# Performance work log

Hardware: AMD Instinct MI355X
Metric: run time of the kernel (lower is better)

The kernel has to match this reference:

```python
import jax, jax.numpy as jnp
import numpy as np

EMBED_DIM = 768
NUM_HEADS = 12
HEAD_DIM = EMBED_DIM // NUM_HEADS
B, N = 4, 2048


def setup_inputs() -> dict:
    key = jax.random.key(0)
    k_x, k_wqkv, k_bqkv, k_wo, k_bo = jax.random.split(key, 5)
    s = 1.0 / np.sqrt(EMBED_DIM)
    return {
        "x": jax.random.normal(k_x, (B, N, EMBED_DIM), dtype=jnp.float32),
        # torch nn.Linear weight layout: [out_features, in_features]
        "w_qkv": jax.random.uniform(k_wqkv, (3 * EMBED_DIM, EMBED_DIM), minval=-s, maxval=s, dtype=jnp.float32),
        "b_qkv": jax.random.uniform(k_bqkv, (3 * EMBED_DIM,), minval=-s, maxval=s, dtype=jnp.float32),
        "w_out": jax.random.uniform(k_wo, (EMBED_DIM, EMBED_DIM), minval=-s, maxval=s, dtype=jnp.float32),
        "b_out": jax.random.uniform(k_bo, (EMBED_DIM,), minval=-s, maxval=s, dtype=jnp.float32),
    }


def reference(x, w_qkv, b_qkv, w_out, b_out):
    Bsz, Nlen, C = x.shape
    # fused QKV projection: [B, N, 3C]
    qkv = jnp.einsum("bnc,oc->bno", x, w_qkv) + b_qkv
    qkv = qkv.reshape(Bsz, Nlen, 3, NUM_HEADS, HEAD_DIM)
    q = qkv[:, :, 0].transpose(0, 2, 1, 3)  # [B, H, N, D]
    k = qkv[:, :, 1].transpose(0, 2, 1, 3)
    v = qkv[:, :, 2].transpose(0, 2, 1, 3)
    scale = 1.0 / np.sqrt(HEAD_DIM).astype(np.float32)
    scores = jnp.einsum("bhqd,bhkd->bhqk", q, k) * scale  # [B, H, N, N]
    attn = jax.nn.softmax(scores, axis=-1)
    ctx = jnp.einsum("bhqk,bhkd->bhqd", attn, v)  # [B, H, N, D]
    ctx = ctx.transpose(0, 2, 1, 3).reshape(Bsz, Nlen, C)
    return jnp.einsum("bnc,oc->bno", ctx, w_out) + b_out
```

## Files before the change

### kernel.cpp

```cpp
#include <hip/hip_runtime.h>
#include <math.h>

typedef __attribute__((ext_vector_type(8))) short bf16x8;
typedef __attribute__((ext_vector_type(4))) short bf16x4;
typedef __attribute__((ext_vector_type(4))) float f32x4;
typedef __attribute__((ext_vector_type(16))) float f32x16;
typedef unsigned short u16;

namespace {
constexpr int BATCH = 4, SEQ = 2048, CDIM = 768, NH = 12, HD = 64;
constexpr int MROWS = BATCH * SEQ;
constexpr int KD = CDIM;
constexpr float QSCALE = 0.125f * 1.44269504088896f;
}

__device__ __forceinline__ u16 f2bf(float f) {
  unsigned x = __float_as_uint(f);
  return (u16)((x + 0x7fffu + ((x >> 16) & 1u)) >> 16);
}

__device__ __forceinline__ unsigned pk2bf(float a, float b) {
  unsigned r;
  asm("v_cvt_pk_bf16_f32 %0, %1, %2" : "=v"(r) : "v"(a), "v"(b));
  return r;
}

#if defined(__has_builtin)
#if __has_builtin(__builtin_amdgcn_exp2f)
#define EXP2(x) __builtin_amdgcn_exp2f(x)
#endif
#endif
#ifndef EXP2
#define EXP2(x) exp2f(x)
#endif

#define GLD16(gp, lp)                                                        \
  __builtin_amdgcn_global_load_lds(                                          \
      (const __attribute__((address_space(1))) void*)(gp),                   \
      (__attribute__((address_space(3))) void*)(lp), 16, 0, 0)

__global__ void convert_bf16(const float* __restrict__ x, u16* __restrict__ xb, int nx4,
                             const float* __restrict__ w1, u16* __restrict__ w1b, int n14,
                             const float* __restrict__ w2, u16* __restrict__ w2b, int n24) {
  const int stride = gridDim.x * blockDim.x;
  const int t0 = blockIdx.x * blockDim.x + threadIdx.x;
  for (int i = t0; i < nx4; i += stride) {
    float4 v = ((const float4*)x)[i];
    ushort4 o; o.x = f2bf(v.x); o.y = f2bf(v.y); o.z = f2bf(v.z); o.w = f2bf(v.w);
    ((ushort4*)xb)[i] = o;
  }
  for (int i = t0; i < n14; i += stride) {
    float4 v = ((const float4*)w1)[i];
    ushort4 o; o.x = f2bf(v.x); o.y = f2bf(v.y); o.z = f2bf(v.z); o.w = f2bf(v.w);
    ((ushort4*)w1b)[i] = o;
  }
  for (int i = t0; i < n24; i += stride) {
    float4 v = ((const float4*)w2)[i];
    ushort4 o; o.x = f2bf(v.x); o.y = f2bf(v.y); o.z = f2bf(v.z); o.w = f2bf(v.w);
    ((ushort4*)w2b)[i] = o;
  }
}

template <int MODE>
__global__ __launch_bounds__(512, 4) void gemm_bf16(
    const u16* __restrict__ A, const u16* __restrict__ Bw,
    const float* __restrict__ bias, float* __restrict__ outf,
    u16* __restrict__ qws, u16* __restrict__ kws, u16* __restrict__ vws) {
  __shared__ u16 smem[2 * 2 * 128 * 64];
  const int t = threadIdx.x;
  const int w = t >> 6, l = t & 63, g = l >> 4, li = l & 15;
  const int wm = w >> 1, wn = w & 1;
  const int lin = blockIdx.x;
  const int rowb = ((lin & 7) << 3) | ((lin >> 3) & 7);
  const int colb = lin >> 6;
  const int row0 = rowb * 128, col0 = colb * 128;

  const int srow = w * 16 + (l >> 3);
  const int skc = (l & 7) ^ (l >> 3);
  const u16* gA = A + (size_t)(row0 + srow) * KD + skc * 8;
  const u16* gB = Bw + (size_t)(col0 + srow) * KD + skc * 8;

  f32x4 acc[2][4];
#pragma unroll
  for (int a = 0; a < 2; ++a)
#pragma unroll
    for (int c = 0; c < 4; ++c) acc[a][c] = {0.f, 0.f, 0.f, 0.f};

#define GSTAGE(kt_, buf_)                                                     \
  do {                                                                        \
    const int k0_ = (kt_) * 64;                                               \
    u16* As_ = smem + (buf_) * (2 * 128 * 64);                                \
    u16* Bs_ = As_ + 128 * 64;                                                \
    _Pragma("unroll")                                                         \
    for (int j = 0; j < 2; ++j) {                                             \
      GLD16(gA + (size_t)8 * j * KD + k0_, &As_[(w * 16 + 8 * j) * 64]);      \
      GLD16(gB + (size_t)8 * j * KD + k0_, &Bs_[(w * 16 + 8 * j) * 64]);      \
    }                                                                         \
  } while (0)

  constexpr int NK = KD / 64;
  GSTAGE(0, 0);
  GSTAGE(1, 1);
  asm volatile("s_waitcnt vmcnt(4)" ::: "memory");
  __builtin_amdgcn_sched_barrier(0);
  __builtin_amdgcn_s_barrier();
  __builtin_amdgcn_sched_barrier(0);

  for (int kt = 0; kt < NK; ++kt) {
    const int cur = kt & 1;
    const u16* AsC = smem + cur * (2 * 128 * 64);
    const u16* BsC = AsC + 128 * 64;

    bf16x8 af[2][2], bfr[4][2];
#pragma unroll
    for (int mi = 0; mi < 2; ++mi) {
      const int r = wm * 32 + mi * 16 + li;
#pragma unroll
      for (int ks = 0; ks < 2; ++ks)
        af[mi][ks] = *(const bf16x8*)&AsC[r * 64 + (((ks * 4 + g) ^ (li & 7)) * 8)];
    }
#pragma unroll
    for (int ni = 0; ni < 4; ++ni) {
      const int r = wn * 64 + ni * 16 + li;
#pragma unroll
      for (int ks = 0; ks < 2; ++ks)
        bfr[ni][ks] = *(const bf16x8*)&BsC[r * 64 + (((ks * 4 + g) ^ (li & 7)) * 8)];
    }
    __builtin_amdgcn_s_setprio(1);
#pragma unroll
    for (int ni = 0; ni < 4; ++ni)
#pragma unroll
      for (int mi = 0; mi < 2; ++mi) {
        acc[mi][ni] = __builtin_amdgcn_mfma_f32_16x16x32_bf16(af[mi][0], bfr[ni][0], acc[mi][ni], 0, 0, 0);
        acc[mi][ni] = __builtin_amdgcn_mfma_f32_16x16x32_bf16(af[mi][1], bfr[ni][1], acc[mi][ni], 0, 0, 0);
      }
    __builtin_amdgcn_s_setprio(0);

    if (kt + 1 < NK) {
      asm volatile("s_waitcnt vmcnt(0)" ::: "memory");
      __builtin_amdgcn_sched_barrier(0);
      __builtin_amdgcn_s_barrier();
      __builtin_amdgcn_sched_barrier(0);
      if (kt + 2 < NK) GSTAGE(kt + 2, cur);
    }
  }
#undef GSTAGE

  float bsr[4];
#pragma unroll
  for (int ni = 0; ni < 4; ++ni) bsr[ni] = bias[col0 + wn * 64 + ni * 16 + li];
  const int bidx = row0 >> 11;
  const int nseq0 = row0 & (SEQ - 1);

  __syncthreads();

  if (MODE == 1) {
    float* Cf = (float*)smem;
#pragma unroll
    for (int p = 0; p < 4; ++p) {
      if (wm == p) {
#pragma unroll
        for (int mi = 0; mi < 2; ++mi)
#pragma unroll
          for (int ni = 0; ni < 4; ++ni)
#pragma unroll
            for (int i = 0; i < 4; ++i)
              Cf[(mi * 16 + 4 * g + i) * 132 + wn * 64 + ni * 16 + li] =
                  acc[mi][ni][i] + bsr[ni];
      }
      __syncthreads();
#pragma unroll
      for (int j = 0; j < 2; ++j) {
        const int fid = t + 512 * j;
        const int r = fid >> 5, c4 = (fid & 31) * 4;
        *(float4*)(outf + (size_t)(row0 + p * 32 + r) * CDIM + col0 + c4) =
            *(const float4*)&Cf[r * 132 + c4];
      }
      __syncthreads();
    }
  } else {
#pragma unroll
    for (int hc = 0; hc < 2; ++hc) {
      const int nb = col0 + hc * 64;
      const int s = nb / CDIM;
      const int h = (nb % CDIM) / HD;
      if (wn == hc) {
        if (s < 2) {
          const float qs = (s == 0) ? QSCALE : 1.f;
#pragma unroll
          for (int mi = 0; mi < 2; ++mi)
#pragma unroll
            for (int ni = 0; ni < 4; ++ni)
#pragma unroll
              for (int i = 0; i < 4; ++i)
                smem[(wm * 32 + mi * 16 + 4 * g + i) * 72 + ni * 16 + li] =
                    f2bf((acc[mi][ni][i] + bsr[ni]) * qs);
        } else {
#pragma unroll
          for (int mi = 0; mi < 2; ++mi)
#pragma unroll
            for (int ni = 0; ni < 4; ++ni)
#pragma unroll
              for (int i = 0; i < 4; ++i)
                smem[(ni * 16 + li) * 136 + wm * 32 + mi * 16 + 4 * g + i] =
                    f2bf(acc[mi][ni][i] + bsr[ni]);
        }
      }
      __syncthreads();
      if (s < 2) {
        u16* dst = (s == 0 ? qws : kws) + ((size_t)(bidx * NH + h) * SEQ + nseq0) * HD;
        const int r = t >> 3, c = (t & 7) * 8;
#pragma unroll
        for (int rd = 0; rd < 2; ++rd)
          *(uint4*)(dst + (size_t)(r + 64 * rd) * HD + c) =
              *(const uint4*)&smem[(r + 64 * rd) * 72 + c];
      } else {
        u16* dst = vws + (size_t)(bidx * NH + h) * HD * SEQ + nseq0;
        const int d = t >> 4, c = (t & 15) * 8;
#pragma unroll
        for (int rd = 0; rd < 2; ++rd)
          *(uint4*)(dst + (size_t)(d + 32 * rd) * SEQ + c) =
              *(const uint4*)&smem[(d + 32 * rd) * 136 + c];
      }
      __syncthreads();
    }
  }
}

__global__ __launch_bounds__(128, 2) void attn_mfma(
    const u16* __restrict__ qws, const u16* __restrict__ kws,
    const u16* __restrict__ vws, u16* __restrict__ ctx) {
  __shared__ u16 smem[4 * 64 * 64];
  u16* Ks0 = smem;
  u16* Vs0 = smem + 2 * 64 * 64;
  const int t = threadIdx.x;
  const int w = t >> 6, l = t & 63;
  const int hi = l >> 5, c = l & 31;
  const int n = blockIdx.x;
  const int xcd = n & 7, j = n >> 3;
  const int hb = xcd * 6 + (j >> 4);
  const int q0 = (j & 15) * 128;
  const int h = hb % NH, b = hb / NH;
  const size_t bh = (size_t)b * NH + h;
  const u16* qbp = qws + bh * SEQ * HD;
  const u16* kb = kws + bh * SEQ * HD;
  const u16* vb = vws + bh * HD * SEQ;
  const int qw = q0 + w * 64;

  bf16x8 qf[2][4];
#pragma unroll
  for (int qt = 0; qt < 2; ++qt)
#pragma unroll
    for (int ks4 = 0; ks4 < 4; ++ks4)
      qf[qt][ks4] = *(const bf16x8*)(qbp + (size_t)(qw + qt * 32 + c) * HD + ks4 * 16 + hi * 8);
  asm volatile("s_waitcnt vmcnt(0)" ::: "memory");
  __builtin_amdgcn_sched_barrier(0);

  f32x16 acc[2][2];
#pragma unroll
  for (int dt = 0; dt < 2; ++dt)
#pragma unroll
    for (int qt = 0; qt < 2; ++qt)
#pragma unroll
      for (int r = 0; r < 16; ++r) acc[dt][qt][r] = 0.f;
  f32x16 Z;
#pragma unroll
  for (int r = 0; r < 16; ++r) Z[r] = 0.f;
  float lrun[2] = {0.f, 0.f};

  const int srow8 = l >> 3;
  const int skc = (l & 7) ^ srow8;
  const u16* gK = kb + (size_t)(w * 32 + srow8) * HD + skc * 8;
  const u16* gV = vb + (size_t)(w * 32 + srow8) * SEQ + skc * 8;

  constexpr int NT = SEQ / 64;

#define STAGE(kt_, buf_)                                                           \
  do {                                                                             \
    const int key0_ = (kt_) * 64;                                                  \
    _Pragma("unroll")                                                              \
    for (int jj = 0; jj < 4; ++jj) {                                               \
      GLD16(gK + (size_t)(key0_ + 8 * jj) * HD, &Ks0[(buf_) * 4096 + (w * 32 + 8 * jj) * 64]); \
      GLD16(gV + (size_t)(8 * jj) * SEQ + key0_, &Vs0[(buf_) * 4096 + (w * 32 + 8 * jj) * 64]); \
    }                                                                              \
  } while (0)

  STAGE(0, 0);
  STAGE(1, 1);
  asm volatile("s_waitcnt vmcnt(8)" ::: "memory");
  __builtin_amdgcn_sched_barrier(0);
  __builtin_amdgcn_s_barrier();
  __builtin_amdgcn_sched_barrier(0);

  for (int kt = 0; kt < NT; ++kt) {
    const int cur = kt & 1;
    const u16* KsC = Ks0 + cur * 4096;
    const u16* VsC = Vs0 + cur * 4096;

#pragma unroll
    for (int kt32 = 0; kt32 < 2; ++kt32) {
      f32x16 S0, S1;
      __builtin_amdgcn_s_setprio(1);
      {
        bf16x8 kf0 = *(const bf16x8*)&KsC[(kt32 * 32 + c) * 64 + (((0 * 2 + hi) ^ (l & 7)) * 8)];
        S0 = __builtin_amdgcn_mfma_f32_32x32x16_bf16(kf0, qf[0][0], Z, 0, 0, 0);
        S1 = __builtin_amdgcn_mfma_f32_32x32x16_bf16(kf0, qf[1][0], Z, 0, 0, 0);
        bf16x8 kf1 = *(const bf16x8*)&KsC[(kt32 * 32 + c) * 64 + (((1 * 2 + hi) ^ (l & 7)) * 8)];
        S0 = __builtin_amdgcn_mfma_f32_32x32x16_bf16(kf1, qf[0][1], S0, 0, 0, 0);
        S1 = __builtin_amdgcn_mfma_f32_32x32x16_bf16(kf1, qf[1][1], S1, 0, 0, 0);
        bf16x8 kf2 = *(const bf16x8*)&KsC[(kt32 * 32 + c) * 64 + (((2 * 2 + hi) ^ (l & 7)) * 8)];
        S0 = __builtin_amdgcn_mfma_f32_32x32x16_bf16(kf2, qf[0][2], S0, 0, 0, 0);
        S1 = __builtin_amdgcn_mfma_f32_32x32x16_bf16(kf2, qf[1][2], S1, 0, 0, 0);
        bf16x8 kf3 = *(const bf16x8*)&KsC[(kt32 * 32 + c) * 64 + (((3 * 2 + hi) ^ (l & 7)) * 8)];
        S0 = __builtin_amdgcn_mfma_f32_32x32x16_bf16(kf3, qf[0][3], S0, 0, 0, 0);
        S1 = __builtin_amdgcn_mfma_f32_32x32x16_bf16(kf3, qf[1][3], S1, 0, 0, 0);
      }
      __builtin_amdgcn_s_setprio(0);

      unsigned W0[4][2], W1[4][2];
#pragma unroll
      for (int qt = 0; qt < 2; ++qt) {
        const f32x16& S = (qt == 0) ? S0 : S1;
        float rs = 0.f;
#pragma unroll
        for (int u = 0; u < 4; ++u) {
          const float p0 = EXP2(S[4 * u + 0]);
          const float p1 = EXP2(S[4 * u + 1]);
          const float p2 = EXP2(S[4 * u + 2]);
          const float p3 = EXP2(S[4 * u + 3]);
          rs += (p0 + p1) + (p2 + p3);
          unsigned lo = pk2bf(p0, p1);
          unsigned hiw = pk2bf(p2, p3);
          if (qt == 0) { W0[u][0] = lo; W0[u][1] = hiw; }
          else         { W1[u][0] = lo; W1[u][1] = hiw; }
        }
        lrun[qt] += rs;
      }

      __builtin_amdgcn_s_setprio(1);
#pragma unroll
      for (int s = 0; s < 2; ++s) {
        union { uint4 u4; bf16x8 v; } p0v, p1v;
        p0v.u4.x = W0[2 * s][0]; p0v.u4.y = W0[2 * s][1];
        p0v.u4.z = W0[2 * s + 1][0]; p0v.u4.w = W0[2 * s + 1][1];
        p1v.u4.x = W1[2 * s][0]; p1v.u4.y = W1[2 * s][1];
        p1v.u4.z = W1[2 * s + 1][0]; p1v.u4.w = W1[2 * s + 1][1];
        const int ck0 = kt32 * 4 + 2 * s;
        const int ck1 = ck0 + 1;
#pragma unroll
        for (int dt = 0; dt < 2; ++dt) {
          const int rowoff = (dt * 32 + c) * 64;
          union { struct { bf16x4 a, b; } p; bf16x8 v; } vfu;
          vfu.p.a = *(const bf16x4*)&VsC[rowoff + ((ck0 ^ (l & 7)) * 8) + hi * 4];
          vfu.p.b = *(const bf16x4*)&VsC[rowoff + ((ck1 ^ (l & 7)) * 8) + hi * 4];
          acc[dt][0] = __builtin_amdgcn_mfma_f32_32x32x16_bf16(vfu.v, p0v.v, acc[dt][0], 0, 0, 0);
          acc[dt][1] = __builtin_amdgcn_mfma_f32_32x32x16_bf16(vfu.v, p1v.v, acc[dt][1], 0, 0, 0);
        }
      }
      __builtin_amdgcn_s_setprio(0);
    }

    if (kt + 1 < NT) {
      asm volatile("s_waitcnt vmcnt(0)" ::: "memory");
      __builtin_amdgcn_sched_barrier(0);
      __builtin_amdgcn_s_barrier();
      __builtin_amdgcn_sched_barrier(0);
      if (kt + 2 < NT) STAGE(kt + 2, cur);
    }
  }
#undef STAGE

  float inv[2];
#pragma unroll
  for (int qt = 0; qt < 2; ++qt) {
    lrun[qt] += __shfl_xor(lrun[qt], 32);
    inv[qt] = 1.f / lrun[qt];
  }
  __syncthreads();
  u16* Os = smem + w * (64 * 72);
#pragma unroll
  for (int qt = 0; qt < 2; ++qt)
#pragma unroll
    for (int dt = 0; dt < 2; ++dt)
#pragma unroll
      for (int u = 0; u < 4; ++u) {
        uint2 pk;
        pk.x = pk2bf(acc[dt][qt][4 * u + 0] * inv[qt], acc[dt][qt][4 * u + 1] * inv[qt]);
        pk.y = pk2bf(acc[dt][qt][4 * u + 2] * inv[qt], acc[dt][qt][4 * u + 3] * inv[qt]);
        const int row = qt * 32 + c;
        const int d0 = dt * 32 + 8 * u + 4 * hi;
        *(uint2*)&Os[row * 72 + d0] = pk;
      }
  asm volatile("s_waitcnt lgkmcnt(0)" ::: "memory");
  __builtin_amdgcn_sched_barrier(0);
  {
    const int rr = l >> 3, cc = (l & 7) * 8;
#pragma unroll
    for (int it = 0; it < 8; ++it) {
      const int row = 8 * it + rr;
      *(uint4*)(ctx + ((size_t)b * SEQ + qw + row) * CDIM + h * HD + cc) =
          *(const uint4*)&Os[row * 72 + cc];
    }
  }
}

extern "C" void kernel_launch(void* const* d_in, const int* in_sizes, int n_in,
                              void* d_out, int out_size, void* d_ws, size_t ws_size,
                              hipStream_t stream) {
  (void)in_sizes; (void)n_in; (void)out_size; (void)ws_size;
  const float* x     = (const float*)d_in[0];
  const float* w_qkv = (const float*)d_in[1];
  const float* b_qkv = (const float*)d_in[2];
  const float* w_out = (const float*)d_in[3];
  const float* b_out = (const float*)d_in[4];
  float* out = (float*)d_out;

  u16* xb    = (u16*)d_ws;
  u16* wqkvb = xb + (size_t)MROWS * KD;
  u16* wob   = wqkvb + (size_t)3 * CDIM * KD;
  u16* qb    = wob + (size_t)CDIM * KD;
  const size_t QS = (size_t)BATCH * NH * SEQ * HD;
  u16* kb   = qb + QS;
  u16* vb   = kb + QS;
  u16* ctxb = vb + QS;

  hipLaunchKernelGGL(convert_bf16, dim3(2048), dim3(256), 0, stream,
                     x, xb, MROWS * KD / 4,
                     w_qkv, wqkvb, 3 * CDIM * KD / 4,
                     w_out, wob, CDIM * KD / 4);
  hipLaunchKernelGGL((gemm_bf16<0>), dim3((MROWS / 128) * (3 * CDIM / 128)), dim3(512), 0,
                     stream, xb, wqkvb, b_qkv, nullptr, qb, kb, vb);
  hipLaunchKernelGGL(attn_mfma, dim3(16 * NH * BATCH), dim3(128), 0, stream,
                     qb, kb, vb, ctxb);
  hipLaunchKernelGGL((gemm_bf16<1>), dim3((MROWS / 128) * (CDIM / 128)), dim3(512), 0,
                     stream, ctxb, wob, b_out, out, nullptr, nullptr, nullptr);
}
```

Measured before the change: 207.6 us.

## Split attention key range across two wave pairs and reduce partials in LDS

The attention kernel goes from 128 to 256 threads per block. Two wave pairs each process half of the key sequence (split-K) for the same 128 queries, and their unnormalized accumulators and row sums are combined through shared memory at the end. Each iteration now handles 32 keys per wave pair instead of 64. The intent is more waves per CU to hide latency and shorter serial loops. The cost is an extra LDS reduction and barriers, plus more per-block register and LDS pressure.

```diff
diff --git a/kernel.cpp b/kernel.cpp
--- a/kernel.cpp
+++ b/kernel.cpp
@@ -227,15 +227,16 @@
   }
 }
 
-__global__ __launch_bounds__(128, 2) void attn_mfma(
+__global__ __launch_bounds__(256, 3) void attn_mfma(
     const u16* __restrict__ qws, const u16* __restrict__ kws,
     const u16* __restrict__ vws, u16* __restrict__ ctx) {
-  __shared__ u16 smem[4 * 64 * 64];
+  __shared__ u16 smem[16896];
   u16* Ks0 = smem;
-  u16* Vs0 = smem + 2 * 64 * 64;
+  u16* Vs0 = smem + 8192;
   const int t = threadIdx.x;
   const int w = t >> 6, l = t & 63;
   const int hi = l >> 5, c = l & 31;
+  const int kh = w >> 1, wq = w & 1;
   const int n = blockIdx.x;
   const int xcd = n & 7, j = n >> 3;
   const int hb = xcd * 6 + (j >> 4);
@@ -245,7 +246,7 @@
   const u16* qbp = qws + bh * SEQ * HD;
   const u16* kb = kws + bh * SEQ * HD;
   const u16* vb = vws + bh * HD * SEQ;
-  const int qw = q0 + w * 64;
+  const int qw = q0 + wq * 64;
 
   bf16x8 qf[2][4];
 #pragma unroll
@@ -270,24 +271,24 @@
 
   const int srow8 = l >> 3;
   const int skc = (l & 7) ^ srow8;
-  const u16* gK = kb + (size_t)(w * 32 + srow8) * HD + skc * 8;
-  const u16* gV = vb + (size_t)(w * 32 + srow8) * SEQ + skc * 8;
-
-  constexpr int NT = SEQ / 64;
-
-#define STAGE(kt_, buf_)                                                           \
+  const u16* gK = kb + (size_t)((w >> 1) * 1024 + (w & 1) * 16 + srow8) * HD + skc * 8;
+  const u16* gV = vb + (size_t)(w * 16 + srow8) * SEQ + (skc >> 2) * 1024 + (skc & 3) * 8;
+
+  constexpr int NT = SEQ / 2 / 32;
+
+#define STAGE(t_, buf_)                                                            \
   do {                                                                             \
-    const int key0_ = (kt_) * 64;                                                  \
+    const int key0_ = (t_) * 32;                                                   \
     _Pragma("unroll")                                                              \
-    for (int jj = 0; jj < 4; ++jj) {                                               \
-      GLD16(gK + (size_t)(key0_ + 8 * jj) * HD, &Ks0[(buf_) * 4096 + (w * 32 + 8 * jj) * 64]); \
-      GLD16(gV + (size_t)(8 * jj) * SEQ + key0_, &Vs0[(buf_) * 4096 + (w * 32 + 8 * jj) * 64]); \
+    for (int jj = 0; jj < 2; ++jj) {                                               \
+      GLD16(gK + (size_t)(key0_ + 8 * jj) * HD, &Ks0[(buf_) * 4096 + (w * 16 + 8 * jj) * 64]); \
+      GLD16(gV + (size_t)(8 * jj) * SEQ + key0_, &Vs0[(buf_) * 4096 + (w * 16 + 8 * jj) * 64]); \
     }                                                                              \
   } while (0)
 
   STAGE(0, 0);
   STAGE(1, 1);
-  asm volatile("s_waitcnt vmcnt(8)" ::: "memory");
+  asm volatile("s_waitcnt vmcnt(4)" ::: "memory");
   __builtin_amdgcn_sched_barrier(0);
   __builtin_amdgcn_s_barrier();
   __builtin_amdgcn_sched_barrier(0);
@@ -297,68 +298,65 @@
     const u16* KsC = Ks0 + cur * 4096;
     const u16* VsC = Vs0 + cur * 4096;
 
-#pragma unroll
-    for (int kt32 = 0; kt32 < 2; ++kt32) {
-      f32x16 S0, S1;
-      __builtin_amdgcn_s_setprio(1);
-      {
-        bf16x8 kf0 = *(const bf16x8*)&KsC[(kt32 * 32 + c) * 64 + (((0 * 2 + hi) ^ (l & 7)) * 8)];
-        S0 = __builtin_amdgcn_mfma_f32_32x32x16_bf16(kf0, qf[0][0], Z, 0, 0, 0);
-        S1 = __builtin_amdgcn_mfma_f32_32x32x16_bf16(kf0, qf[1][0], Z, 0, 0, 0);
-        bf16x8 kf1 = *(const bf16x8*)&KsC[(kt32 * 32 + c) * 64 + (((1 * 2 + hi) ^ (l & 7)) * 8)];
-        S0 = __builtin_amdgcn_mfma_f32_32x32x16_bf16(kf1, qf[0][1], S0, 0, 0, 0);
-        S1 = __builtin_amdgcn_mfma_f32_32x32x16_bf16(kf1, qf[1][1], S1, 0, 0, 0);
-        bf16x8 kf2 = *(const bf16x8*)&KsC[(kt32 * 32 + c) * 64 + (((2 * 2 + hi) ^ (l & 7)) * 8)];
-        S0 = __builtin_amdgcn_mfma_f32_32x32x16_bf16(kf2, qf[0][2], S0, 0, 0, 0);
-        S1 = __builtin_amdgcn_mfma_f32_32x32x16_bf16(kf2, qf[1][2], S1, 0, 0, 0);
-        bf16x8 kf3 = *(const bf16x8*)&KsC[(kt32 * 32 + c) * 64 + (((3 * 2 + hi) ^ (l & 7)) * 8)];
-        S0 = __builtin_amdgcn_mfma_f32_32x32x16_bf16(kf3, qf[0][3], S0, 0, 0, 0);
-        S1 = __builtin_amdgcn_mfma_f32_32x32x16_bf16(kf3, qf[1][3], S1, 0, 0, 0);
-      }
-      __builtin_amdgcn_s_setprio(0);
-
-      unsigned W0[4][2], W1[4][2];
-#pragma unroll
-      for (int qt = 0; qt < 2; ++qt) {
-        const f32x16& S = (qt == 0) ? S0 : S1;
-        float rs = 0.f;
-#pragma unroll
-        for (int u = 0; u < 4; ++u) {
-          const float p0 = EXP2(S[4 * u + 0]);
-          const float p1 = EXP2(S[4 * u + 1]);
-          const float p2 = EXP2(S[4 * u + 2]);
-          const float p3 = EXP2(S[4 * u + 3]);
-          rs += (p0 + p1) + (p2 + p3);
-          unsigned lo = pk2bf(p0, p1);
-          unsigned hiw = pk2bf(p2, p3);
-          if (qt == 0) { W0[u][0] = lo; W0[u][1] = hiw; }
-          else         { W1[u][0] = lo; W1[u][1] = hiw; }
-        }
-        lrun[qt] += rs;
-      }
-
-      __builtin_amdgcn_s_setprio(1);
-#pragma unroll
-      for (int s = 0; s < 2; ++s) {
-        union { uint4 u4; bf16x8 v; } p0v, p1v;
-        p0v.u4.x = W0[2 * s][0]; p0v.u4.y = W0[2 * s][1];
-        p0v.u4.z = W0[2 * s + 1][0]; p0v.u4.w = W0[2 * s + 1][1];
-        p1v.u4.x = W1[2 * s][0]; p1v.u4.y = W1[2 * s][1];
-        p1v.u4.z = W1[2 * s + 1][0]; p1v.u4.w = W1[2 * s + 1][1];
-        const int ck0 = kt32 * 4 + 2 * s;
-        const int ck1 = ck0 + 1;
-#pragma unroll
-        for (int dt = 0; dt < 2; ++dt) {
-          const int rowoff = (dt * 32 + c) * 64;
-          union { struct { bf16x4 a, b; } p; bf16x8 v; } vfu;
-          vfu.p.a = *(const bf16x4*)&VsC[rowoff + ((ck0 ^ (l & 7)) * 8) + hi * 4];
-          vfu.p.b = *(const bf16x4*)&VsC[rowoff + ((ck1 ^ (l & 7)) * 8) + hi * 4];
-          acc[dt][0] = __builtin_amdgcn_mfma_f32_32x32x16_bf16(vfu.v, p0v.v, acc[dt][0], 0, 0, 0);
-          acc[dt][1] = __builtin_amdgcn_mfma_f32_32x32x16_bf16(vfu.v, p1v.v, acc[dt][1], 0, 0, 0);
-        }
-      }
-      __builtin_amdgcn_s_setprio(0);
-    }
+    f32x16 S0, S1;
+    __builtin_amdgcn_s_setprio(1);
+    {
+      bf16x8 kf0 = *(const bf16x8*)&KsC[(kh * 32 + c) * 64 + (((0 * 2 + hi) ^ (l & 7)) * 8)];
+      S0 = __builtin_amdgcn_mfma_f32_32x32x16_bf16(kf0, qf[0][0], Z, 0, 0, 0);
+      S1 = __builtin_amdgcn_mfma_f32_32x32x16_bf16(kf0, qf[1][0], Z, 0, 0, 0);
+      bf16x8 kf1 = *(const bf16x8*)&KsC[(kh * 32 + c) * 64 + (((1 * 2 + hi) ^ (l & 7)) * 8)];
+      S0 = __builtin_amdgcn_mfma_f32_32x32x16_bf16(kf1, qf[0][1], S0, 0, 0, 0);
+      S1 = __builtin_amdgcn_mfma_f32_32x32x16_bf16(kf1, qf[1][1], S1, 0, 0, 0);
+      bf16x8 kf2 = *(const bf16x8*)&KsC[(kh * 32 + c) * 64 + (((2 * 2 + hi) ^ (l & 7)) * 8)];
+      S0 = __builtin_amdgcn_mfma_f32_32x32x16_bf16(kf2, qf[0][2], S0, 0, 0, 0);
+      S1 = __builtin_amdgcn_mfma_f32_32x32x16_bf16(kf2, qf[1][2], S1, 0, 0, 0);
+      bf16x8 kf3 = *(const bf16x8*)&KsC[(kh * 32 + c) * 64 + (((3 * 2 + hi) ^ (l & 7)) * 8)];
+      S0 = __builtin_amdgcn_mfma_f32_32x32x16_bf16(kf3, qf[0][3], S0, 0, 0, 0);
+      S1 = __builtin_amdgcn_mfma_f32_32x32x16_bf16(kf3, qf[1][3], S1, 0, 0, 0);
+    }
+    __builtin_amdgcn_s_setprio(0);
+
+    unsigned W0[4][2], W1[4][2];
+#pragma unroll
+    for (int qt = 0; qt < 2; ++qt) {
+      const f32x16& S = (qt == 0) ? S0 : S1;
+      float rs = 0.f;
+#pragma unroll
+      for (int u = 0; u < 4; ++u) {
+        const float p0 = EXP2(S[4 * u + 0]);
+        const float p1 = EXP2(S[4 * u + 1]);
+        const float p2 = EXP2(S[4 * u + 2]);
+        const float p3 = EXP2(S[4 * u + 3]);
+        rs += (p0 + p1) + (p2 + p3);
+        unsigned lo = pk2bf(p0, p1);
+        unsigned hiw = pk2bf(p2, p3);
+        if (qt == 0) { W0[u][0] = lo; W0[u][1] = hiw; }
+        else         { W1[u][0] = lo; W1[u][1] = hiw; }
+      }
+      lrun[qt] += rs;
+    }
+
+    __builtin_amdgcn_s_setprio(1);
+#pragma unroll
+    for (int s = 0; s < 2; ++s) {
+      union { uint4 u4; bf16x8 v; } p0v, p1v;
+      p0v.u4.x = W0[2 * s][0]; p0v.u4.y = W0[2 * s][1];
+      p0v.u4.z = W0[2 * s + 1][0]; p0v.u4.w = W0[2 * s + 1][1];
+      p1v.u4.x = W1[2 * s][0]; p1v.u4.y = W1[2 * s][1];
+      p1v.u4.z = W1[2 * s + 1][0]; p1v.u4.w = W1[2 * s + 1][1];
+      const int ck0 = kh * 4 + 2 * s;
+      const int ck1 = ck0 + 1;
+#pragma unroll
+      for (int dt = 0; dt < 2; ++dt) {
+        const int rowoff = (dt * 32 + c) * 64;
+        union { struct { bf16x4 a, b; } p; bf16x8 v; } vfu;
+        vfu.p.a = *(const bf16x4*)&VsC[rowoff + ((ck0 ^ (l & 7)) * 8) + hi * 4];
+        vfu.p.b = *(const bf16x4*)&VsC[rowoff + ((ck1 ^ (l & 7)) * 8) + hi * 4];
+        acc[dt][0] = __builtin_amdgcn_mfma_f32_32x32x16_bf16(vfu.v, p0v.v, acc[dt][0], 0, 0, 0);
+        acc[dt][1] = __builtin_amdgcn_mfma_f32_32x32x16_bf16(vfu.v, p1v.v, acc[dt][1], 0, 0, 0);
+      }
+    }
+    __builtin_amdgcn_s_setprio(0);
 
     if (kt + 1 < NT) {
       asm volatile("s_waitcnt vmcnt(0)" ::: "memory");
@@ -370,30 +368,56 @@
   }
 #undef STAGE
 
-  float inv[2];
-#pragma unroll
-  for (int qt = 0; qt < 2; ++qt) {
-    lrun[qt] += __shfl_xor(lrun[qt], 32);
-    inv[qt] = 1.f / lrun[qt];
-  }
   __syncthreads();
-  u16* Os = smem + w * (64 * 72);
-#pragma unroll
-  for (int qt = 0; qt < 2; ++qt)
+  float* cbf = (float*)smem;
+  float* cbl = (float*)(smem + 16384);
+  if (kh == 1) {
 #pragma unroll
     for (int dt = 0; dt < 2; ++dt)
 #pragma unroll
-      for (int u = 0; u < 4; ++u) {
-        uint2 pk;
-        pk.x = pk2bf(acc[dt][qt][4 * u + 0] * inv[qt], acc[dt][qt][4 * u + 1] * inv[qt]);
-        pk.y = pk2bf(acc[dt][qt][4 * u + 2] * inv[qt], acc[dt][qt][4 * u + 3] * inv[qt]);
-        const int row = qt * 32 + c;
-        const int d0 = dt * 32 + 8 * u + 4 * hi;
-        *(uint2*)&Os[row * 72 + d0] = pk;
-      }
-  asm volatile("s_waitcnt lgkmcnt(0)" ::: "memory");
-  __builtin_amdgcn_sched_barrier(0);
-  {
+      for (int qt = 0; qt < 2; ++qt)
+#pragma unroll
+        for (int r = 0; r < 16; ++r)
+          cbf[wq * 4096 + (dt * 2 + qt) * 1024 + r * 64 + l] = acc[dt][qt][r];
+    cbl[wq * 128 + l] = lrun[0];
+    cbl[wq * 128 + 64 + l] = lrun[1];
+  }
+  __syncthreads();
+  if (kh == 0) {
+#pragma unroll
+    for (int dt = 0; dt < 2; ++dt)
+#pragma unroll
+      for (int qt = 0; qt < 2; ++qt)
+#pragma unroll
+        for (int r = 0; r < 16; ++r)
+          acc[dt][qt][r] += cbf[wq * 4096 + (dt * 2 + qt) * 1024 + r * 64 + l];
+    lrun[0] += cbl[wq * 128 + l];
+    lrun[1] += cbl[wq * 128 + 64 + l];
+  }
+  __syncthreads();
+  if (kh == 0) {
+    float inv[2];
+#pragma unroll
+    for (int qt = 0; qt < 2; ++qt) {
+      lrun[qt] += __shfl_xor(lrun[qt], 32);
+      inv[qt] = 1.f / lrun[qt];
+    }
+    u16* Os = smem + wq * 4608;
+#pragma unroll
+    for (int qt = 0; qt < 2; ++qt)
+#pragma unroll
+      for (int dt = 0; dt < 2; ++dt)
+#pragma unroll
+        for (int u = 0; u < 4; ++u) {
+          uint2 pk;
+          pk.x = pk2bf(acc[dt][qt][4 * u + 0] * inv[qt], acc[dt][qt][4 * u + 1] * inv[qt]);
+          pk.y = pk2bf(acc[dt][qt][4 * u + 2] * inv[qt], acc[dt][qt][4 * u + 3] * inv[qt]);
+          const int row = qt * 32 + c;
+          const int d0 = dt * 32 + 8 * u + 4 * hi;
+          *(uint2*)&Os[row * 72 + d0] = pk;
+        }
+    asm volatile("s_waitcnt lgkmcnt(0)" ::: "memory");
+    __builtin_amdgcn_sched_barrier(0);
     const int rr = l >> 3, cc = (l & 7) * 8;
 #pragma unroll
     for (int it = 0; it < 8; ++it) {
@@ -430,7 +454,7 @@
                      w_out, wob, CDIM * KD / 4);
   hipLaunchKernelGGL((gemm_bf16<0>), dim3((MROWS / 128) * (3 * CDIM / 128)), dim3(512), 0,
                      stream, xb, wqkvb, b_qkv, nullptr, qb, kb, vb);
-  hipLaunchKernelGGL(attn_mfma, dim3(16 * NH * BATCH), dim3(128), 0, stream,
+  hipLaunchKernelGGL(attn_mfma, dim3(16 * NH * BATCH), dim3(256), 0, stream,
                      qb, kb, vb, ctxb);
   hipLaunchKernelGGL((gemm_bf16<1>), dim3((MROWS / 128) * (CDIM / 128)), dim3(512), 0,
                      stream, ctxb, wob, b_out, out, nullptr, nullptr, nullptr);
```

Result: no change. 204.9 us (-1.3%).
